# Kernel optimization log

Hardware: AMD Instinct MI355X
Metric: run time of the kernel (lower is better)

## Reference

```python
import jax, jax.numpy as jnp
import numpy as np

_SIGMA = 1.5
_K1 = 0.01
_K2 = 0.03
WINDOW_SIZE = 11
VALUE_RANGE = 1.0


def gaussian_window(size: int, sigma: float) -> jnp.ndarray:
    # 1D gaussian, normalized; 2D window is the outer product (sums to 1)
    coords = jnp.arange(size, dtype=jnp.float32) - (size - 1) / 2.0
    g = jnp.exp(-(coords ** 2) / (2.0 * sigma ** 2))
    g = g / g.sum()
    return jnp.outer(g, g)  # (k, k)


def depthwise_conv(img, win2d):
    # img: (N, C, H, W), win2d: (k, k); depthwise valid conv, groups=C
    C = img.shape[1]
    kern = jnp.broadcast_to(win2d[:, :, None, None], win2d.shape + (1, C))  # HWIO
    return jax.lax.conv_general_dilated(
        img, kern, window_strides=(1, 1), padding='VALID',
        dimension_numbers=('NCHW', 'HWIO', 'NCHW'), feature_group_count=C)


def setup_inputs() -> dict:
    key = jax.random.key(0)
    k1, k2 = jax.random.split(key)
    x = jax.random.uniform(k1, (16, 3, 512, 512), dtype=jnp.float32)
    y = jax.random.uniform(k2, (16, 3, 512, 512), dtype=jnp.float32)
    window = gaussian_window(WINDOW_SIZE, _SIGMA)
    return {'x': x, 'y': y, 'window': window}


def reference(x, y, window):
    mu_x = depthwise_conv(x, window)
    mu_y = depthwise_conv(y, window)
    mu_x_sq = mu_x ** 2
    mu_y_sq = mu_y ** 2
    mu_xy = mu_x * mu_y
    sigma_x_sq = depthwise_conv(x * x, window) - mu_x_sq
    sigma_y_sq = depthwise_conv(y * y, window) - mu_y_sq
    sigma_xy = depthwise_conv(x * y, window) - mu_xy
    c1 = (_K1 * VALUE_RANGE) ** 2
    c2 = (_K2 * VALUE_RANGE) ** 2
    cs_map = (2.0 * sigma_xy + c2) / (sigma_x_sq + sigma_y_sq + c2)
    ssim_map = (2.0 * mu_xy + c1) / (mu_x_sq + mu_y_sq + c1) * cs_map
    # mean over spatial dims -> (N, C), mean over channels -> (N,), reduction='mean' -> scalar
    return ssim_map.mean(axis=(-1, -2)).mean(axis=-1).mean()
```

## Files before the change

### kernel.cpp

```cpp
#include <hip/hip_runtime.h>
#include <math.h>

#define KS    11
#define H     512
#define W     512
#define OH    502
#define OW    502
#define NPLANES 48
#define TOTAL_OUT (NPLANES * OH * OW)

#define TH      4
#define IROWS   (TH + KS - 1)
#define LVWP    523
#define NTHREADS 512
#define CHUNK   24
#define NCHUNKS 21

typedef float v2f __attribute__((ext_vector_type(2)));

__global__ void zero_out_kernel(float* out) { out[0] = 0.0f; }

__device__ __forceinline__ float uniform_f(float v) {
    return __int_as_float(__builtin_amdgcn_readfirstlane(__float_as_int(v)));
}

__global__ __launch_bounds__(NTHREADS, 4) void ssim_kernel(
    const float* __restrict__ x,
    const float* __restrict__ y,
    const float* __restrict__ win,
    float* __restrict__ out)
{
    __shared__ v2f vp[2][TH][LVWP];
    __shared__ float w1s[KS];
    __shared__ float wsum[NTHREADS / 64];

    const int t     = threadIdx.x;
    const int chunk = blockIdx.x;
    const int plane = blockIdx.y;

    const int row_lo = chunk * CHUNK;
    const int row_hi = (row_lo + CHUNK < OH) ? (row_lo + CHUNK) : OH;
    const int niter  = (row_hi - row_lo + TH - 1) / TH;

    const float* __restrict__ xp = x + (size_t)plane * (H * W);
    const float* __restrict__ yp = y + (size_t)plane * (H * W);

    if (t < KS) w1s[t] = sqrtf(win[t * KS + t]);
    __syncthreads();

    float w[KS];
#pragma unroll
    for (int k = 0; k < KS; k++) w[k] = uniform_f(w1s[k]);

    const int r  = t & 3;
    const int c0 = (t >> 2) << 2;
    const float c1 = 1e-4f;
    const float c2 = 9e-4f;
    float acc = 0.f;

    float rx[IROWS], ry[IROWS];
#pragma unroll
    for (int j = 0; j < IROWS; j++) {
        int gy = row_lo + j; gy = (gy < H - 1) ? gy : (H - 1);
        rx[j] = xp[gy * W + t];
        ry[j] = yp[gy * W + t];
    }

    for (int it = 0; it < niter; ++it) {
        const int gy0 = row_lo + it * TH;

        v2f A[TH], B[TH];
#pragma unroll
        for (int q = 0; q < TH; q++) { A[q] = (v2f){0.f, 0.f}; B[q] = (v2f){0.f, 0.f}; }

#pragma unroll
        for (int j = 0; j < IROWS; j++) {
            const float xv = rx[j], yv = ry[j];
            const v2f d0 = {xv, yv};
            const v2f d1 = {xv * xv + yv * yv, xv * yv};
#pragma unroll
            for (int q = 0; q < TH; q++) {
                if (j - q >= 0 && j - q < KS) {
                    const float wk = w[j - q];
                    A[q] += wk * d0;
                    B[q] += wk * d1;
                }
            }
        }

        __syncthreads();
#pragma unroll
        for (int q = 0; q < TH; q++) {
            vp[0][q][t] = A[q];
            vp[1][q][t] = B[q];
        }
        __syncthreads();

        if (it + 1 < niter) {
#pragma unroll
            for (int j = 0; j < IROWS - TH; j++) {
                rx[j] = rx[j + TH];
                ry[j] = ry[j + TH];
            }
#pragma unroll
            for (int j = 0; j < TH; j++) {
                int gy = gy0 + IROWS + j;
                gy = (gy < H - 1) ? gy : (H - 1);
                rx[IROWS - TH + j] = xp[gy * W + t];
                ry[IROWS - TH + j] = yp[gy * W + t];
            }
        }

        v2f M0[TH], M1[TH];
#pragma unroll
        for (int p = 0; p < TH; p++) { M0[p] = (v2f){0.f, 0.f}; M1[p] = (v2f){0.f, 0.f}; }

#pragma unroll
        for (int k = 0; k < IROWS; k++) {
            const v2f p0 = vp[0][r][c0 + k];
            const v2f p1 = vp[1][r][c0 + k];
#pragma unroll
            for (int p = 0; p < TH; p++) {
                if (k - p >= 0 && k - p < KS) {
                    const float wk = w[k - p];
                    M0[p] += wk * p0;
                    M1[p] += wk * p1;
                }
            }
        }

        const int grow  = gy0 + r;
        const bool rowok = (grow < row_hi);
#pragma unroll
        for (int p = 0; p < TH; p++) {
            if (rowok && (c0 + p) < OW) {
                const float mux = M0[p][0], muy = M0[p][1];
                const float mxy = mux * muy;
                const float m2  = mux * mux + muy * muy;
                const float sss = M1[p][0] - m2;
                const float sxy = M1[p][1] - mxy;
                const float num = (2.f * sxy + c2) * (2.f * mxy + c1);
                const float den = (sss + c2) * (m2 + c1);
                acc += num * __builtin_amdgcn_rcpf(den);
            }
        }
    }

#pragma unroll
    for (int off = 32; off > 0; off >>= 1)
        acc += __shfl_down(acc, off, 64);

    if ((t & 63) == 0) wsum[t >> 6] = acc;
    __syncthreads();
    if (t == 0) {
        float s = 0.f;
#pragma unroll
        for (int i = 0; i < NTHREADS / 64; i++) s += wsum[i];
        atomicAdd(out, s * (1.0f / (float)TOTAL_OUT));
    }
}

extern "C" void kernel_launch(void* const* d_in, const int* in_sizes, int n_in,
                              void* d_out, int out_size, void* d_ws, size_t ws_size,
                              hipStream_t stream)
{
    const float* x   = (const float*)d_in[0];
    const float* y   = (const float*)d_in[1];
    const float* win = (const float*)d_in[2];
    float* out = (float*)d_out;

    zero_out_kernel<<<1, 1, 0, stream>>>(out);

    dim3 grid(NCHUNKS, NPLANES);
    ssim_kernel<<<grid, NTHREADS, 0, stream>>>(x, y, win, out);
}
```

Before: 141.2 us.

## Give each wave its own column strip and LDS slab, removing block barriers

Work is repartitioned so each 64-lane wave handles a 64-column strip (54 valid outputs) over 32 rows. Each wave gets a private LDS slab, so the two __syncthreads per iteration are dropped; ordering within a single wave keeps the LDS write/read correct. The cost is horizontal halo redundancy (64 columns loaded for 54 outputs) and 8 idle lanes in the horizontal pass. Vertical halo overhead per row falls because each wave now covers more rows.

```diff
diff --git a/kernel.cpp b/kernel.cpp
--- a/kernel.cpp
+++ b/kernel.cpp
@@ -11,10 +11,13 @@
 
 #define TH      4
 #define IROWS   (TH + KS - 1)
-#define LVWP    523
+#define SCOLS   64
+#define SOUT    54
+#define LVWS    67
+#define NSTRIPS 10
 #define NTHREADS 512
-#define CHUNK   24
-#define NCHUNKS 21
+#define WCHUNK  32
+#define NITER   8
 
 typedef float v2f __attribute__((ext_vector_type(2)));
 
@@ -30,17 +33,23 @@
     const float* __restrict__ win,
     float* __restrict__ out)
 {
-    __shared__ v2f vp[2][TH][LVWP];
+    __shared__ v2f vp[NTHREADS / 64][2][TH][LVWS];
     __shared__ float w1s[KS];
     __shared__ float wsum[NTHREADS / 64];
 
-    const int t     = threadIdx.x;
-    const int chunk = blockIdx.x;
+    const int t   = threadIdx.x;
+    const int l   = t & 63;
+    const int wid = t >> 6;
+
+    const int sh    = blockIdx.x;
+    const int strip = sh % NSTRIPS;
+    const int half  = sh / NSTRIPS;
     const int plane = blockIdx.y;
 
-    const int row_lo = chunk * CHUNK;
-    const int row_hi = (row_lo + CHUNK < OH) ? (row_lo + CHUNK) : OH;
-    const int niter  = (row_hi - row_lo + TH - 1) / TH;
+    const int col_base = strip * SOUT;
+    int gxi = col_base + l;
+    const int gx = (gxi < W) ? gxi : (W - 1);
+    const int row_lo = half * 256 + wid * WCHUNK;
 
     const float* __restrict__ xp = x + (size_t)plane * (H * W);
     const float* __restrict__ yp = y + (size_t)plane * (H * W);
@@ -52,21 +61,25 @@
 #pragma unroll
     for (int k = 0; k < KS; k++) w[k] = uniform_f(w1s[k]);
 
-    const int r  = t & 3;
-    const int c0 = (t >> 2) << 2;
+    const int r  = l & 3;
+    const int u  = l >> 2;
+    const bool lane_ok = (u <= 13);
+    const int c0 = lane_ok ? (u << 2) : 40;
     const float c1 = 1e-4f;
     const float c2 = 9e-4f;
     float acc = 0.f;
 
+    v2f (* __restrict__ sl)[TH][LVWS] = vp[wid];
+
     float rx[IROWS], ry[IROWS];
 #pragma unroll
     for (int j = 0; j < IROWS; j++) {
-        int gy = row_lo + j; gy = (gy < H - 1) ? gy : (H - 1);
-        rx[j] = xp[gy * W + t];
-        ry[j] = yp[gy * W + t];
+        const int gy = row_lo + j;
+        rx[j] = xp[gy * W + gx];
+        ry[j] = yp[gy * W + gx];
     }
 
-    for (int it = 0; it < niter; ++it) {
+    for (int it = 0; it < NITER; ++it) {
         const int gy0 = row_lo + it * TH;
 
         v2f A[TH], B[TH];
@@ -88,15 +101,13 @@
             }
         }
 
-        __syncthreads();
 #pragma unroll
         for (int q = 0; q < TH; q++) {
-            vp[0][q][t] = A[q];
-            vp[1][q][t] = B[q];
+            sl[0][q][l] = A[q];
+            sl[1][q][l] = B[q];
         }
-        __syncthreads();
 
-        if (it + 1 < niter) {
+        if (it + 1 < NITER) {
 #pragma unroll
             for (int j = 0; j < IROWS - TH; j++) {
                 rx[j] = rx[j + TH];
@@ -106,8 +117,8 @@
             for (int j = 0; j < TH; j++) {
                 int gy = gy0 + IROWS + j;
                 gy = (gy < H - 1) ? gy : (H - 1);
-                rx[IROWS - TH + j] = xp[gy * W + t];
-                ry[IROWS - TH + j] = yp[gy * W + t];
+                rx[IROWS - TH + j] = xp[gy * W + gx];
+                ry[IROWS - TH + j] = yp[gy * W + gx];
             }
         }
 
@@ -117,8 +128,8 @@
 
 #pragma unroll
         for (int k = 0; k < IROWS; k++) {
-            const v2f p0 = vp[0][r][c0 + k];
-            const v2f p1 = vp[1][r][c0 + k];
+            const v2f p0 = sl[0][r][c0 + k];
+            const v2f p1 = sl[1][r][c0 + k];
 #pragma unroll
             for (int p = 0; p < TH; p++) {
                 if (k - p >= 0 && k - p < KS) {
@@ -129,11 +140,11 @@
             }
         }
 
-        const int grow  = gy0 + r;
-        const bool rowok = (grow < row_hi);
+        const int grow = gy0 + r;
 #pragma unroll
         for (int p = 0; p < TH; p++) {
-            if (rowok && (c0 + p) < OW) {
+            const int lc = c0 + p;
+            if (lane_ok && grow < OH && lc < SOUT && (col_base + lc) < OW) {
                 const float mux = M0[p][0], muy = M0[p][1];
                 const float mxy = mux * muy;
                 const float m2  = mux * mux + muy * muy;
@@ -150,7 +161,7 @@
     for (int off = 32; off > 0; off >>= 1)
         acc += __shfl_down(acc, off, 64);
 
-    if ((t & 63) == 0) wsum[t >> 6] = acc;
+    if (l == 0) wsum[wid] = acc;
     __syncthreads();
     if (t == 0) {
         float s = 0.f;
@@ -171,6 +182,6 @@
 
     zero_out_kernel<<<1, 1, 0, stream>>>(out);
 
-    dim3 grid(NCHUNKS, NPLANES);
+    dim3 grid(NSTRIPS * 2, NPLANES);
     ssim_kernel<<<grid, NTHREADS, 0, stream>>>(x, y, win, out);
 }
```

Result: slower. 146.3 us (+3.6%).

## Double-buffer vertical-pass LDS tiles and double the rows per block

Applied to the files above, without the earlier changes.

Splits the shared vertical-pass buffer into two halves so the next tile's vertical convolution and global loads overlap the current tile's horizontal pass. This cuts the syncs per iteration from two to one. Each block now covers 48 output rows instead of 24, which reduces the halo rows reloaded per block. In exchange it doubles LDS use per block, lowers the occupancy hint to 3, and produces fewer blocks (11x48), which may underfill the GPU.

```diff
diff --git a/kernel.cpp b/kernel.cpp
--- a/kernel.cpp
+++ b/kernel.cpp
@@ -13,8 +13,8 @@
 #define IROWS   (TH + KS - 1)
 #define LVWP    523
 #define NTHREADS 512
-#define CHUNK   24
-#define NCHUNKS 21
+#define CHUNK   48
+#define NCHUNKS 11
 
 typedef float v2f __attribute__((ext_vector_type(2)));
 
@@ -24,13 +24,13 @@
     return __int_as_float(__builtin_amdgcn_readfirstlane(__float_as_int(v)));
 }
 
-__global__ __launch_bounds__(NTHREADS, 4) void ssim_kernel(
+__global__ __launch_bounds__(NTHREADS, 3) void ssim_kernel(
     const float* __restrict__ x,
     const float* __restrict__ y,
     const float* __restrict__ win,
     float* __restrict__ out)
 {
-    __shared__ v2f vp[2][TH][LVWP];
+    __shared__ v2f vp[2][2][TH][LVWP];
     __shared__ float w1s[KS];
     __shared__ float wsum[NTHREADS / 64];
 
@@ -61,18 +61,15 @@
     float rx[IROWS], ry[IROWS];
 #pragma unroll
     for (int j = 0; j < IROWS; j++) {
-        int gy = row_lo + j; gy = (gy < H - 1) ? gy : (H - 1);
+        const int gy = row_lo + j;
         rx[j] = xp[gy * W + t];
         ry[j] = yp[gy * W + t];
     }
 
-    for (int it = 0; it < niter; ++it) {
-        const int gy0 = row_lo + it * TH;
-
+    {
         v2f A[TH], B[TH];
 #pragma unroll
         for (int q = 0; q < TH; q++) { A[q] = (v2f){0.f, 0.f}; B[q] = (v2f){0.f, 0.f}; }
-
 #pragma unroll
         for (int j = 0; j < IROWS; j++) {
             const float xv = rx[j], yv = ry[j];
@@ -87,38 +84,34 @@
                 }
             }
         }
+#pragma unroll
+        for (int q = 0; q < TH; q++) { vp[0][0][q][t] = A[q]; vp[0][1][q][t] = B[q]; }
+    }
+    __syncthreads();
 
-        __syncthreads();
-#pragma unroll
-        for (int q = 0; q < TH; q++) {
-            vp[0][q][t] = A[q];
-            vp[1][q][t] = B[q];
-        }
-        __syncthreads();
+    int cur = 0;
+    for (int it = 0; it < niter; ++it) {
+        const int gy0 = row_lo + it * TH;
+        const bool more = (it + 1 < niter);
 
-        if (it + 1 < niter) {
-#pragma unroll
-            for (int j = 0; j < IROWS - TH; j++) {
-                rx[j] = rx[j + TH];
-                ry[j] = ry[j + TH];
-            }
+        float ntx[TH], nty[TH];
+        if (more) {
 #pragma unroll
             for (int j = 0; j < TH; j++) {
                 int gy = gy0 + IROWS + j;
                 gy = (gy < H - 1) ? gy : (H - 1);
-                rx[IROWS - TH + j] = xp[gy * W + t];
-                ry[IROWS - TH + j] = yp[gy * W + t];
+                ntx[j] = xp[gy * W + t];
+                nty[j] = yp[gy * W + t];
             }
         }
 
         v2f M0[TH], M1[TH];
 #pragma unroll
         for (int p = 0; p < TH; p++) { M0[p] = (v2f){0.f, 0.f}; M1[p] = (v2f){0.f, 0.f}; }
-
 #pragma unroll
         for (int k = 0; k < IROWS; k++) {
-            const v2f p0 = vp[0][r][c0 + k];
-            const v2f p1 = vp[1][r][c0 + k];
+            const v2f p0 = vp[cur][0][r][c0 + k];
+            const v2f p1 = vp[cur][1][r][c0 + k];
 #pragma unroll
             for (int p = 0; p < TH; p++) {
                 if (k - p >= 0 && k - p < KS) {
@@ -127,6 +120,33 @@
                     M1[p] += wk * p1;
                 }
             }
+        }
+
+        if (more) {
+#pragma unroll
+            for (int j = 0; j < IROWS - TH; j++) { rx[j] = rx[j + TH]; ry[j] = ry[j + TH]; }
+#pragma unroll
+            for (int j = 0; j < TH; j++) { rx[IROWS - TH + j] = ntx[j]; ry[IROWS - TH + j] = nty[j]; }
+
+            v2f A[TH], B[TH];
+#pragma unroll
+            for (int q = 0; q < TH; q++) { A[q] = (v2f){0.f, 0.f}; B[q] = (v2f){0.f, 0.f}; }
+#pragma unroll
+            for (int j = 0; j < IROWS; j++) {
+                const float xv = rx[j], yv = ry[j];
+                const v2f d0 = {xv, yv};
+                const v2f d1 = {xv * xv + yv * yv, xv * yv};
+#pragma unroll
+                for (int q = 0; q < TH; q++) {
+                    if (j - q >= 0 && j - q < KS) {
+                        const float wk = w[j - q];
+                        A[q] += wk * d0;
+                        B[q] += wk * d1;
+                    }
+                }
+            }
+#pragma unroll
+            for (int q = 0; q < TH; q++) { vp[cur ^ 1][0][q][t] = A[q]; vp[cur ^ 1][1][q][t] = B[q]; }
         }
 
         const int grow  = gy0 + r;
@@ -144,6 +164,9 @@
                 acc += num * __builtin_amdgcn_rcpf(den);
             }
         }
+
+        if (more) __syncthreads();
+        cur ^= 1;
     }
 
 #pragma unroll
```

New measurement: 148.9 us. 5.5% more time.
